# Kernel tuning notes

Hardware: AMD Instinct MI355X
Metric: run time of the kernel (lower is better)

## Reference

```python
import jax, jax.numpy as jnp
import numpy as np

EPS = 1e-5  # PNA std-aggregator epsilon
N_NODES, N_EDGES, F_DIM, N_LAYERS = 50000, 800000, 64, 3


def setup_inputs() -> dict:
    key = jax.random.key(0)
    ks = jax.random.split(key, 6)
    x = jax.random.normal(ks[0], (N_NODES, F_DIM), jnp.float32)
    edge_index = jax.random.randint(ks[1], (2, N_EDGES), 0, N_NODES, jnp.int32)
    # Per-layer parameters, stacked on a leading layer axis.
    pre_w = jax.random.normal(ks[2], (N_LAYERS, 2 * F_DIM, F_DIM), jnp.float32) / np.sqrt(2 * F_DIM).astype(np.float32)
    pre_b = jnp.zeros((N_LAYERS, F_DIM), jnp.float32)
    post_w = jax.random.normal(ks[3], (N_LAYERS, 13 * F_DIM, F_DIM), jnp.float32) / np.sqrt(13 * F_DIM).astype(np.float32)
    post_b = jnp.zeros((N_LAYERS, F_DIM), jnp.float32)
    lin_w = jax.random.normal(ks[4], (N_LAYERS, F_DIM, F_DIM), jnp.float32) / np.sqrt(F_DIM).astype(np.float32)
    lin_b = jnpp = jnp.zeros((N_LAYERS, F_DIM), jnp.float32)
    return dict(x=x, edge_index=edge_index, pre_w=pre_w, pre_b=pre_b,
                post_w=post_w, post_b=post_b, lin_w=lin_w, lin_b=lin_b)


def reference(x, edge_index, pre_w, pre_b, post_w, post_b, lin_w, lin_b):
    src, dst = edge_index[0], edge_index[1]
    n = x.shape[0]
    # In-degree of aggregation targets (clamped to >=1, as in PyG DegreeScalerAggregation).
    deg = jax.ops.segment_sum(jnp.ones_like(dst, dtype=x.dtype), dst, num_segments=n)
    has_edge = (deg > 0)[:, None]
    deg_c = jnp.maximum(deg, 1.0)[:, None]              # [N,1]
    log_deg = jnp.log(deg_c + 1.0)                      # [N,1]
    avg_log = jnp.mean(log_deg)
    amp = log_deg / avg_log                              # amplification scaler
    att = avg_log / log_deg                              # attenuation scaler

    h = x
    for l in range(pre_w.shape[0]):
        # message: pre_nn(cat([x_i, x_j]))  -> [E, F]
        m = jnp.concatenate([h[dst], h[src]], axis=-1) @ pre_w[l] + pre_b[l]
        # fused multi-aggregator scatter-reduce per target node
        s1 = jax.ops.segment_sum(m, dst, num_segments=n)
        s2 = jax.ops.segment_sum(m * m, dst, num_segments=n)
        mean = s1 / deg_c
        std = jnp.sqrt(jax.nn.relu(s2 / deg_c - mean * mean) + EPS)
        mx = jnp.where(has_edge, jax.ops.segment_max(m, dst, num_segments=n), 0.0)
        mn = jnp.where(has_edge, jax.ops.segment_min(m, dst, num_segments=n), 0.0)
        agg = jnp.concatenate([mean, mx, mn, std], axis=-1)        # [N, 4F]
        scaled = jnp.concatenate([agg, agg * amp, agg * att], -1)  # [N, 12F]
        # post_nn(cat([x, scaled])) then final lin, plus residual shortcut
        out = jnp.concatenate([h, scaled], axis=-1) @ post_w[l] + post_b[l]
        out = out @ lin_w[l] + lin_b[l]
        h = out + h
    return h
```

## Files before the change

kernel.cpp:

```cpp
#include <hip/hip_runtime.h>
#include <math.h>

#define EPSV 1e-5f
#define EPB3 4096
#define NBP 256
#define CAP 6144
#define CAPS (CAP + 768)

typedef short s16x8 __attribute__((ext_vector_type(8)));
typedef float f32x4 __attribute__((ext_vector_type(4)));
typedef unsigned short u16;
typedef unsigned short u16x4 __attribute__((ext_vector_type(4)));

#define MFMA(a, b, c) __builtin_amdgcn_mfma_f32_16x16x32_bf16(a, b, c, 0, 0, 0)

__device__ inline u16 f2bf(float f) {
    unsigned u = __float_as_uint(f);
    return (u16)((u + 0x7FFF + ((u >> 16) & 1)) >> 16);
}
__device__ inline float bf2f(u16 h) { return __uint_as_float(((unsigned)h) << 16); }

__device__ inline void split8(const float4& a, const float4& b, s16x8& hv, s16x8& lv) {
    float f[8] = {a.x, a.y, a.z, a.w, b.x, b.y, b.z, b.w};
#pragma unroll
    for (int i = 0; i < 8; ++i) {
        u16 h = f2bf(f[i]);
        hv[i] = (short)h;
        lv[i] = (short)f2bf(f[i] - bf2f(h));
    }
}


__global__ void k_wprep(const float* __restrict__ pre_w, const float* __restrict__ post_w,
                        const float* __restrict__ post_b, const float* __restrict__ lin_w,
                        const float* __restrict__ lin_b, u16* __restrict__ WpT_hi,
                        u16* __restrict__ WpT_lo, u16* __restrict__ WT_hi,
                        u16* __restrict__ WT_lo, float* __restrict__ bpp,
                        int* __restrict__ bucketCur, float* __restrict__ lsum) {
    int l = blockIdx.y, bx = blockIdx.x, t = threadIdx.x;
    if (bx < 320) {
        int k = bx, j = t;
        int third = j >> 6, c = j & 63;
        float out = 0.f;
        int r = -1;
        if (k < 64) r = (third == 0) ? k : -1;
        else        r = 64 + third * 256 + (k - 64);
        if (r >= 0) {
            const float* pw = post_w + (size_t)(l * 832 + r) * 64;
            const float* lw = lin_w + (size_t)l * 64 * 64;
            float s = 0.f;
            for (int kk = 0; kk < 64; ++kk) s += pw[kk] * lw[kk * 64 + c];
            out = s;
        }
        u16 h = f2bf(out);
        size_t o = ((size_t)l * 192 + j) * 320 + k;
        WT_hi[o] = h;
        WT_lo[o] = f2bf(out - bf2f(h));
    } else if (bx < 448) {
        if (t < 64) {
            int c = bx - 320, k = t;
            float v = pre_w[(size_t)l * 8192 + (size_t)(k + (c >= 64 ? 64 : 0)) * 64 + (c & 63)];
            u16 h = f2bf(v);
            size_t o = ((size_t)l * 128 + c) * 64 + k;
            WpT_hi[o] = h;
            WpT_lo[o] = f2bf(v - bf2f(h));
        }
    } else if (bx == 448) {
        if (t < 64) {
            int c = t;
            const float* pb = post_b + l * 64;
            const float* lw = lin_w + (size_t)l * 64 * 64;
            float s = lin_b[l * 64 + c];
            for (int k = 0; k < 64; ++k) s += pb[k] * lw[k * 64 + c];
            bpp[l * 64 + c] = s;
        }
    } else if (l == 0) {
        int i = (bx - 449) * 192 + t;
        if (i < NBP) bucketCur[i] = 0;
        if (i == 0) *lsum = 0.f;
    }
}

__global__ __launch_bounds__(512) void k_bucket3(const int* __restrict__ src,
                                                 const int* __restrict__ dst, int E,
                                                 int* __restrict__ bucketCursor,
                                                 unsigned* __restrict__ edgeTmp) {
    __shared__ int cnt[NBP], loff[NBP], lpos[NBP], gbase[NBP], sbuf[NBP];
    __shared__ unsigned stage[EPB3];
    int t = threadIdx.x;
    int base = blockIdx.x * EPB3;
    int cntE = min(EPB3, E - base);
    if (t < NBP) cnt[t] = 0;
    __syncthreads();
    unsigned ed[8];
#pragma unroll
    for (int j = 0; j < 8; ++j) {
        int idx = j * 512 + t;
        if (idx < cntE) {
            int e = base + idx;
            unsigned s = (unsigned)src[e];
            unsigned d = (unsigned)dst[e];
            ed[j] = ((d >> 8) << 24) | ((d & 255u) << 16) | s;
            atomicAdd(&cnt[d >> 8], 1);
        } else ed[j] = 0xFFFFFFFFu;
    }
    __syncthreads();
    if (t < NBP) sbuf[t] = cnt[t];
    __syncthreads();
    for (int o = 1; o < NBP; o <<= 1) {
        int v = 0;
        if (t < NBP && t >= o) v = sbuf[t - o];
        __syncthreads();
        if (t < NBP) sbuf[t] += v;
        __syncthreads();
    }
    if (t < NBP) {
        loff[t] = sbuf[t] - cnt[t];
        lpos[t] = sbuf[t] - cnt[t];
        gbase[t] = (cnt[t] > 0) ? atomicAdd(&bucketCursor[t], cnt[t]) : 0;
    }
    __syncthreads();
#pragma unroll
    for (int j = 0; j < 8; ++j) {
        if (ed[j] != 0xFFFFFFFFu) {
            int b = ed[j] >> 24;
            int p = atomicAdd(&lpos[b], 1);
            stage[p] = ed[j];
        }
    }
    __syncthreads();
    for (int i = t; i < cntE; i += 512) {
        unsigned pr = stage[i];
        int b = pr >> 24;
        int pos = gbase[b] + (i - loff[b]);
        if (pos < CAP) edgeTmp[(size_t)b * CAP + pos] = pr;
    }
}

__global__ __launch_bounds__(512) void k_csort2(const unsigned* __restrict__ edgeTmp,
                                                const int* __restrict__ bucketCur,
                                                int* __restrict__ deg,
                                                int* __restrict__ offs,
                                                float* __restrict__ lsum,
                                                u16* __restrict__ srcSorted,
                                                int N, int E, int NB) {
    __shared__ int scnt[NBP], sbuf[NBP], lcur[NBP], lofs[NBP];
    __shared__ float fred[256];
    __shared__ u16 stageSrc[CAPS];
    __shared__ int cntPs;
    int b = blockIdx.x, t = threadIdx.x;
    int n0 = b << 8;
    int nodes = min(256, N - n0);
    if (t < NBP) { lcur[t] = 0; scnt[t] = 0; }
    __syncthreads();
    int cnt = min(bucketCur[b], CAP);
    const unsigned* ebase = edgeTmp + (size_t)b * CAP;
    for (int i = t; i < cnt; i += 512) atomicAdd(&lcur[(ebase[i] >> 16) & 255], 1);
    __syncthreads();
    float ls = 0.f;
    int d = 0, dP = 0;
    if (t < nodes) {
        d = lcur[t];
        deg[n0 + t] = d;
        ls = logf(fmaxf((float)d, 1.f) + 1.f);
        dP = (d + 3) & ~3;
    }
    if (t < 256) fred[t] = ls;
    if (t < NBP) sbuf[t] = dP;
    __syncthreads();
    for (int o = 1; o < NBP; o <<= 1) {
        int v = 0;
        if (t < NBP && t >= o) v = sbuf[t - o];
        __syncthreads();
        if (t < NBP) sbuf[t] += v;
        __syncthreads();
    }
    if (t < NBP) lofs[t] = sbuf[t] - dP;
    if (t < nodes) offs[n0 + t] = b * CAPS + (sbuf[t] - dP);
    if (t == NBP - 1) cntPs = sbuf[t];
    __syncthreads();
    for (int o = 128; o > 0; o >>= 1) {
        if (t < o) fred[t] += fred[t + o];
        __syncthreads();
    }
    if (t == 0) atomicAdd(lsum, fred[0]);
    for (int i = t; i < cnt; i += 512) {
        unsigned p = ebase[i];
        int dl = (p >> 16) & 255;
        int r = atomicAdd(&scnt[dl], 1);
        stageSrc[lofs[dl] + r] = (u16)(p & 0xFFFFu);
    }
    __syncthreads();
    if (t < nodes && (d & 3)) {
        int lp = lofs[t];
        u16 lastv = stageSrc[lp + d - 1];
        for (int k = d; k < dP; ++k) stageSrc[lp + k] = lastv;
    }
    __syncthreads();
    int cntP = cntPs;
    for (int i = t; i < cntP; i += 512) srcSorted[(size_t)b * CAPS + i] = stageSrc[i];
}


__global__ __launch_bounds__(256) void k_gemm1(const float* __restrict__ h,
                                               const u16* __restrict__ WpT_hi,
                                               const u16* __restrict__ WpT_lo,
                                               const float* __restrict__ pre_b,
                                               u16* __restrict__ Ph, u16* __restrict__ Qh,
                                               int M) {
    __shared__ u16 Ah[64 * 72], Al[64 * 72];
    __shared__ u16 Bh[128 * 72], Bl[128 * 72];
    int t = threadIdx.x, wid = t >> 6, lane = t & 63;
    int rows0 = blockIdx.x * 64;
    int quad = lane >> 4, l16 = lane & 15;
    int wm = wid & 1, wn = wid >> 1;

#pragma unroll
    for (int it = 0; it < 2; ++it) {
        int task = it * 256 + t;
        int r = task >> 3, seg = task & 7;
        int row = rows0 + r;
        float4 v0 = make_float4(0.f, 0.f, 0.f, 0.f), v1 = v0;
        if (row < M) {
            v0 = *(const float4*)&h[(size_t)row * 64 + seg * 8];
            v1 = *(const float4*)&h[(size_t)row * 64 + seg * 8 + 4];
        }
        s16x8 hv, lv;
        split8(v0, v1, hv, lv);
        *(s16x8*)&Ah[r * 72 + seg * 8] = hv;
        *(s16x8*)&Al[r * 72 + seg * 8] = lv;
    }
#pragma unroll
    for (int it = 0; it < 4; ++it) {
        int task = it * 256 + t;
        int c = task >> 3, seg = task & 7;
        *(s16x8*)&Bh[c * 72 + seg * 8] = *(const s16x8*)&WpT_hi[(size_t)c * 64 + seg * 8];
        *(s16x8*)&Bl[c * 72 + seg * 8] = *(const s16x8*)&WpT_lo[(size_t)c * 64 + seg * 8];
    }
    __syncthreads();

    f32x4 acc[2][4];
#pragma unroll
    for (int mt = 0; mt < 2; ++mt)
#pragma unroll
        for (int tt = 0; tt < 4; ++tt) acc[mt][tt] = (f32x4){0.f, 0.f, 0.f, 0.f};

#pragma unroll
    for (int c = 0; c < 2; ++c) {
        s16x8 ah[2], al[2];
#pragma unroll
        for (int mt = 0; mt < 2; ++mt) {
            int r = wm * 32 + mt * 16 + l16;
            ah[mt] = *(s16x8*)&Ah[r * 72 + c * 32 + quad * 8];
            al[mt] = *(s16x8*)&Al[r * 72 + c * 32 + quad * 8];
        }
#pragma unroll
        for (int tt = 0; tt < 4; ++tt) {
            int cc = wn * 64 + tt * 16 + l16;
            s16x8 bh = *(s16x8*)&Bh[cc * 72 + c * 32 + quad * 8];
            s16x8 bl = *(s16x8*)&Bl[cc * 72 + c * 32 + quad * 8];
#pragma unroll
            for (int mt = 0; mt < 2; ++mt) {
                acc[mt][tt] = MFMA(ah[mt], bh, acc[mt][tt]);
                acc[mt][tt] = MFMA(ah[mt], bl, acc[mt][tt]);
                if (wn == 0) acc[mt][tt] = MFMA(al[mt], bh, acc[mt][tt]);
            }
        }
    }

#pragma unroll
    for (int mt = 0; mt < 2; ++mt)
#pragma unroll
        for (int tt = 0; tt < 4; ++tt) {
            int col = wn * 64 + tt * 16 + l16;
#pragma unroll
            for (int r = 0; r < 4; ++r) {
                int row = rows0 + wm * 32 + mt * 16 + quad * 4 + r;
                if (row >= M) continue;
                float v = acc[mt][tt][r];
                if (col < 64) Ph[(size_t)row * 64 + col] = f2bf(v + pre_b[col]);
                else          Qh[(size_t)row * 64 + (col - 64)] = f2bf(v);
            }
        }
}

__global__ __launch_bounds__(256) void k_agg(const u16* __restrict__ Ph,
                                             const u16* __restrict__ Qh,
                                             const int* __restrict__ offs,
                                             const int* __restrict__ degp,
                                             const u16* __restrict__ ss,
                                             u16* __restrict__ AGGh, int N) {
    int w = threadIdx.x >> 6, lane = threadIdx.x & 63;
    int g = lane >> 4;
    int f4b = (lane & 15) << 3;
    int node = blockIdx.x * 16 + w * 4 + g;
    int nc = min(node, N - 1);
    int beg = offs[nc];
    int d = (node < N) ? degp[nc] : 0;
    int dP = (d + 3) & ~3;
    int end = beg + dP;
    int mdP = dP;
    mdP = max(mdP, __shfl_xor(mdP, 16));
    mdP = max(mdP, __shfl_xor(mdP, 32));
    int trips = mdP >> 2;

    float sum0 = 0.f, sum1 = 0.f, sum2 = 0.f, sum3 = 0.f;
    float sq0 = 0.f, sq1 = 0.f, sq2 = 0.f, sq3 = 0.f;
    float mx0 = -3.4e38f, mx1 = -3.4e38f, mx2 = -3.4e38f, mx3 = -3.4e38f;
    float mn0 = 3.4e38f, mn1 = 3.4e38f, mn2 = 3.4e38f, mn3 = 3.4e38f;

    const char* qbase = (const char*)Qh;

#define ACC4(LO, HI)                                                        \
    {                                                                       \
        float q0 = __uint_as_float((LO) << 16);                             \
        float q1 = __uint_as_float((LO) & 0xFFFF0000u);                     \
        float q2 = __uint_as_float((HI) << 16);                             \
        float q3 = __uint_as_float((HI) & 0xFFFF0000u);                     \
        sum0 += q0; sq0 = fmaf(q0, q0, sq0);                                \
        mx0 = fmaxf(mx0, q0); mn0 = fminf(mn0, q0);                         \
        sum1 += q1; sq1 = fmaf(q1, q1, sq1);                                \
        mx1 = fmaxf(mx1, q1); mn1 = fminf(mn1, q1);                         \
        sum2 += q2; sq2 = fmaf(q2, q2, sq2);                                \
        mx2 = fmaxf(mx2, q2); mn2 = fminf(mn2, q2);                         \
        sum3 += q3; sq3 = fmaf(q3, q3, sq3);                                \
        mx3 = fmaxf(mx3, q3); mn3 = fminf(mn3, q3);                         \
    }

    int e = beg;
    for (int it = 0; it < trips; ++it, e += 4) {
        if (e < end) {
            uint2 sw = *(const uint2*)(ss + e);
            unsigned a0 = ((sw.x & 0xFFFFu) << 7) | (unsigned)f4b;
            unsigned a1 = ((sw.x >> 16) << 7) | (unsigned)f4b;
            unsigned a2 = ((sw.y & 0xFFFFu) << 7) | (unsigned)f4b;
            unsigned a3 = ((sw.y >> 16) << 7) | (unsigned)f4b;
            uint2 qa = *(const uint2*)(qbase + a0);
            uint2 qb = *(const uint2*)(qbase + a1);
            uint2 qc = *(const uint2*)(qbase + a2);
            uint2 qd = *(const uint2*)(qbase + a3);
            ACC4(qa.x, qa.y);
            ACC4(qb.x, qb.y);
            ACC4(qc.x, qc.y);
            ACC4(qd.x, qd.y);
        }
    }
#undef ACC4

    if (d & 3) {
        unsigned sl = ss[beg + d - 1];
        uint2 ql = *(const uint2*)(qbase + ((sl << 7) | (unsigned)f4b));
        float padf = (float)(dP - d);
        float qL0 = __uint_as_float(ql.x << 16);
        float qL1 = __uint_as_float(ql.x & 0xFFFF0000u);
        float qL2 = __uint_as_float(ql.y << 16);
        float qL3 = __uint_as_float(ql.y & 0xFFFF0000u);
        float t0 = padf * qL0, t1 = padf * qL1, t2 = padf * qL2, t3 = padf * qL3;
        sum0 -= t0; sq0 = fmaf(-t0, qL0, sq0);
        sum1 -= t1; sq1 = fmaf(-t1, qL1, sq1);
        sum2 -= t2; sq2 = fmaf(-t2, qL2, sq2);
        sum3 -= t3; sq3 = fmaf(-t3, qL3, sq3);
    }

    float dc = fmaxf((float)d, 1.f);
    float inv = 1.0f / dc;
    float e0 = sum0 * inv, e1 = sum1 * inv, e2 = sum2 * inv, e3 = sum3 * inv;
    float sd0 = sqrtf(fmaxf(fmaf(-e0, e0, sq0 * inv), 0.f) + EPSV);
    float sd1 = sqrtf(fmaxf(fmaf(-e1, e1, sq1 * inv), 0.f) + EPSV);
    float sd2 = sqrtf(fmaxf(fmaf(-e2, e2, sq2 * inv), 0.f) + EPSV);
    float sd3 = sqrtf(fmaxf(fmaf(-e3, e3, sq3 * inv), 0.f) + EPSV);

    uint2 pw = *(const uint2*)((const char*)Ph + (((unsigned)nc << 7) | (unsigned)f4b));
    float p0 = __uint_as_float(pw.x << 16), p1 = __uint_as_float(pw.x & 0xFFFF0000u);
    float p2 = __uint_as_float(pw.y << 16), p3 = __uint_as_float(pw.y & 0xFFFF0000u);

    bool he = d > 0;
    float m0 = he ? p0 + e0 : 0.f, m1 = he ? p1 + e1 : 0.f;
    float m2 = he ? p2 + e2 : 0.f, m3 = he ? p3 + e3 : 0.f;
    float X0 = he ? p0 + mx0 : 0.f, X1 = he ? p1 + mx1 : 0.f;
    float X2 = he ? p2 + mx2 : 0.f, X3 = he ? p3 + mx3 : 0.f;
    float n0 = he ? p0 + mn0 : 0.f, n1 = he ? p1 + mn1 : 0.f;
    float n2 = he ? p2 + mn2 : 0.f, n3 = he ? p3 + mn3 : 0.f;

    if (node < N) {
        u16* out = (u16*)((char*)AGGh + (((unsigned)node << 9) | (unsigned)f4b));
        *(u16x4*)(out)       = (u16x4){f2bf(m0), f2bf(m1), f2bf(m2), f2bf(m3)};
        *(u16x4*)(out + 64)  = (u16x4){f2bf(X0), f2bf(X1), f2bf(X2), f2bf(X3)};
        *(u16x4*)(out + 128) = (u16x4){f2bf(n0), f2bf(n1), f2bf(n2), f2bf(n3)};
        *(u16x4*)(out + 192) = (u16x4){f2bf(sd0), f2bf(sd1), f2bf(sd2), f2bf(sd3)};
    }
}

__global__ __launch_bounds__(512) void k_gemm2(const float* __restrict__ hIn,
                                               const u16* __restrict__ AGGh,
                                               const u16* __restrict__ WT_hi,
                                               const u16* __restrict__ WT_lo,
                                               const float* __restrict__ bpp,
                                               const int* __restrict__ degp,
                                               const float* __restrict__ lsum,
                                               float* __restrict__ hOut,
                                               int doNext,
                                               const u16* __restrict__ WpN_hi,
                                               const u16* __restrict__ WpN_lo,
                                               const float* __restrict__ pre_bN,
                                               u16* __restrict__ PhN,
                                               u16* __restrict__ QhN, int M) {
    __shared__ u16 Ah[128 * 40], Al[128 * 40];
    __shared__ u16 Bh[192 * 40], Bl[192 * 40];
    int t = threadIdx.x, wid = t >> 6, lane = t & 63;
    int rows0 = blockIdx.x * 128;
    int quad = lane >> 4, l16 = lane & 15;
    int wm = wid & 3, wn = wid >> 2;

    f32x4 acc[2][6];
#pragma unroll
    for (int mt = 0; mt < 2; ++mt)
#pragma unroll
        for (int tt = 0; tt < 6; ++tt) acc[mt][tt] = (f32x4){0.f, 0.f, 0.f, 0.f};

#pragma unroll
    for (int chunk = 0; chunk < 2; ++chunk) {
        {
            int r = t >> 2, seg = t & 3;
            int row = rows0 + r;
            float4 v0 = make_float4(0.f, 0.f, 0.f, 0.f), v1 = v0;
            if (row < M) {
                v0 = *(const float4*)&hIn[(size_t)row * 64 + chunk * 32 + seg * 8];
                v1 = *(const float4*)&hIn[(size_t)row * 64 + chunk * 32 + seg * 8 + 4];
            }
            s16x8 hv, lv;
            split8(v0, v1, hv, lv);
            *(s16x8*)&Ah[r * 40 + seg * 8] = hv;
            *(s16x8*)&Al[r * 40 + seg * 8] = lv;
        }
        if (t < 256) {
            int c = t >> 2, seg = t & 3;
            int k0g = chunk * 32;
            *(s16x8*)&Bh[c * 40 + seg * 8] = *(const s16x8*)&WT_hi[(size_t)c * 320 + k0g + seg * 8];
            *(s16x8*)&Bl[c * 40 + seg * 8] = *(const s16x8*)&WT_lo[(size_t)c * 320 + k0g + seg * 8];
        }
        __syncthreads();

        s16x8 ah[2], al[2];
#pragma unroll
        for (int mt = 0; mt < 2; ++mt) {
            int r = wm * 32 + mt * 16 + l16;
            ah[mt] = *(s16x8*)&Ah[r * 40 + quad * 8];
            al[mt] = *(s16x8*)&Al[r * 40 + quad * 8];
        }
#pragma unroll
        for (int cg = 0; cg < 2; ++cg) {
            int cc = wn * 32 + cg * 16 + l16;
            s16x8 bh = *(s16x8*)&Bh[cc * 40 + quad * 8];
            s16x8 bl = *(s16x8*)&Bl[cc * 40 + quad * 8];
#pragma unroll
            for (int mt = 0; mt < 2; ++mt) {
                acc[mt][cg] = MFMA(ah[mt], bh, acc[mt][cg]);
                acc[mt][cg] = MFMA(al[mt], bh, acc[mt][cg]);
                acc[mt][cg] = MFMA(ah[mt], bl, acc[mt][cg]);
            }
        }
        __syncthreads();
    }

    for (int chunk = 0; chunk < 8; ++chunk) {
        {
            int r = t >> 2, seg = t & 3;
            int row = rows0 + r;
            s16x8 v = (s16x8){0, 0, 0, 0, 0, 0, 0, 0};
            if (row < M) v = *(const s16x8*)&AGGh[(size_t)row * 256 + chunk * 32 + seg * 8];
            *(s16x8*)&Ah[r * 40 + seg * 8] = v;
        }
        {
            int k0g = 64 + chunk * 32;
#pragma unroll
            for (int it = 0; it < 2; ++it) {
                int task = it * 512 + t;
                if (task < 768) {
                    int c = task >> 2, seg = task & 3;
                    *(s16x8*)&Bh[c * 40 + seg * 8] = *(const s16x8*)&WT_hi[(size_t)c * 320 + k0g + seg * 8];
                    *(s16x8*)&Bl[c * 40 + seg * 8] = *(const s16x8*)&WT_lo[(size_t)c * 320 + k0g + seg * 8];
                }
            }
        }
        __syncthreads();

        s16x8 ah[2];
#pragma unroll
        for (int mt = 0; mt < 2; ++mt) {
            int r = wm * 32 + mt * 16 + l16;
            ah[mt] = *(s16x8*)&Ah[r * 40 + quad * 8];
        }
#pragma unroll
        for (int tt = 0; tt < 6; ++tt) {
            int cc = wn * 32 + (tt & 1) * 16 + (tt >> 1) * 64 + l16;
// ... 63 lines not shown
                            Al[rl * 40 + lc] = f2bf(v - bf2f(hi));
                        }
                    }
            }
            __syncthreads();

            s16x8 ah[2], al[2];
#pragma unroll
            for (int mt = 0; mt < 2; ++mt) {
                int r = wm * 32 + mt * 16 + l16;
                ah[mt] = *(s16x8*)&Ah[r * 40 + quad * 8];
                al[mt] = *(s16x8*)&Al[r * 40 + quad * 8];
            }
#pragma unroll
            for (int tt = 0; tt < 4; ++tt) {
                int cc = wn * 64 + tt * 16 + l16;
                s16x8 bh = *(s16x8*)&Bh[cc * 40 + quad * 8];
                s16x8 bl = *(s16x8*)&Bl[cc * 40 + quad * 8];
#pragma unroll
                for (int mt = 0; mt < 2; ++mt) {
                    acc2[mt][tt] = MFMA(ah[mt], bh, acc2[mt][tt]);
                    acc2[mt][tt] = MFMA(ah[mt], bl, acc2[mt][tt]);
                    if (wn == 0) acc2[mt][tt] = MFMA(al[mt], bh, acc2[mt][tt]);
                }
            }
            __syncthreads();
        }

#pragma unroll
        for (int mt = 0; mt < 2; ++mt)
#pragma unroll
            for (int tt = 0; tt < 4; ++tt) {
                int col = wn * 64 + tt * 16 + l16;
#pragma unroll
                for (int r = 0; r < 4; ++r) {
                    int row = rows0 + wm * 32 + mt * 16 + quad * 4 + r;
                    if (row >= M) continue;
                    float v = acc2[mt][tt][r];
                    if (col < 64) PhN[(size_t)row * 64 + col] = f2bf(v + pre_bN[col]);
                    else          QhN[(size_t)row * 64 + (col - 64)] = f2bf(v);
                }
            }
    }
}


extern "C" void kernel_launch(void* const* d_in, const int* in_sizes, int n_in,
                              void* d_out, int out_size, void* d_ws, size_t ws_size,
                              hipStream_t stream) {
    const float* x      = (const float*)d_in[0];
    const int*   ei     = (const int*)d_in[1];
    const float* pre_w  = (const float*)d_in[2];
    const float* pre_b  = (const float*)d_in[3];
    const float* post_w = (const float*)d_in[4];
    const float* post_b = (const float*)d_in[5];
    const float* lin_w  = (const float*)d_in[6];
    const float* lin_b  = (const float*)d_in[7];

    const int N = in_sizes[0] / 64;
    const int E = in_sizes[1] / 2;
    const int L = in_sizes[2] / (128 * 64);

    const int* srcIdx = ei;
    const int* dstIdx = ei + E;

    char* ws = (char*)d_ws;
    size_t off = 0;
    auto alloc = [&](size_t bytes) {
        void* p = ws + off;
        off += (bytes + 255) & ~(size_t)255;
        return p;
    };
    int*      deg        = (int*)alloc((size_t)N * 4);
    int*      offs       = (int*)alloc((size_t)(N + 1) * 4);
    u16*      srcSorted  = (u16*)alloc((size_t)NBP * CAPS * 2);
    unsigned* edgeTmp    = (unsigned*)alloc((size_t)NBP * CAP * 4);
    int*      bucketCur  = (int*)alloc(NBP * 4);
    float*    lsum       = (float*)alloc(256);
    u16*      WpT_hi     = (u16*)alloc((size_t)L * 128 * 64 * 2);
    u16*      WpT_lo     = (u16*)alloc((size_t)L * 128 * 64 * 2);
    u16*      WT_hi      = (u16*)alloc((size_t)L * 192 * 320 * 2);
    u16*      WT_lo      = (u16*)alloc((size_t)L * 192 * 320 * 2);
    float*    bpp        = (float*)alloc((size_t)L * 64 * 4);
    u16*      Ph         = (u16*)alloc((size_t)N * 64 * 2);
    u16*      Qh         = (u16*)alloc((size_t)N * 64 * 2);
    u16*      AGGh       = (u16*)alloc((size_t)N * 256 * 2);
    float*    hA         = (float*)alloc((size_t)N * 64 * 4);
    float*    hB         = (float*)alloc((size_t)N * 64 * 4);
    (void)ws_size;

    int NB = (N + 255) >> 8;
    int NB1 = (E + EPB3 - 1) / EPB3;
    int initBlk = (NBP + 191) / 192;

    k_wprep<<<dim3(449 + initBlk, L), 192, 0, stream>>>(
        pre_w, post_w, post_b, lin_w, lin_b, WpT_hi, WpT_lo, WT_hi, WT_lo, bpp,
        bucketCur, lsum);
    k_bucket3<<<NB1, 512, 0, stream>>>(srcIdx, dstIdx, E, bucketCur, edgeTmp);
    k_csort2<<<NB, 512, 0, stream>>>(edgeTmp, bucketCur, deg, offs, lsum,
                                     srcSorted, N, E, NB);

    int gblk = (N + 63) / 64;
    int gblk2 = (N + 127) / 128;
    k_gemm1<<<gblk, 256, 0, stream>>>(x, WpT_hi, WpT_lo, pre_b, Ph, Qh, N);

    const float* hIn = x;
    float* hbuf[2] = {hA, hB};
    for (int l = 0; l < L; ++l) {
        float* hOut = (l == L - 1) ? (float*)d_out : hbuf[l & 1];
        int dn = (l < L - 1) ? 1 : 0;
        int ln = dn ? (l + 1) : 0;
        k_agg<<<(N + 15) / 16, 256, 0, stream>>>(Ph, Qh, offs, deg, srcSorted, AGGh, N);
        k_gemm2<<<gblk2, 512, 0, stream>>>(hIn, AGGh,
                                           WT_hi + (size_t)l * 192 * 320,
                                           WT_lo + (size_t)l * 192 * 320,
                                           bpp + (size_t)l * 64,
                                           deg, lsum, hOut, dn,
                                           WpT_hi + (size_t)ln * 128 * 64,
                                           WpT_lo + (size_t)ln * 128 * 64,
                                           pre_b + (size_t)ln * 64,
                                           Ph, Qh, N);
        hIn = hOut;
    }
}
```

Measured before the change: 277.0 us.

## Fuse aggregation into per-layer GEMM kernel and merge preprocessing launches

Each layer's edge aggregation is folded into the post-GEMM kernel, so every 128-node block gathers its own neighbors, writes the aggregated features, then runs the GEMM. The Ph/Qh buffers are double-buffered because the next layer's projections are written while other blocks may still be reading the current ones. Weight prep and edge bucketing are merged into one launch, and CSR sort and the first projection GEMM into another, with memsets replacing the init blocks. This cuts launch count and inter-kernel gaps, but the gather now shares a kernel with the GEMM, which may raise register and LDS pressure and lower occupancy. It also relies on AGGh rows written within a block being visible to that same block's GEMM.

```diff
diff --git a/kernel.cpp b/kernel.cpp
--- a/kernel.cpp
+++ b/kernel.cpp
@@ -10,7 +10,6 @@
 typedef short s16x8 __attribute__((ext_vector_type(8)));
 typedef float f32x4 __attribute__((ext_vector_type(4)));
 typedef unsigned short u16;
-typedef unsigned short u16x4 __attribute__((ext_vector_type(4)));
 
 #define MFMA(a, b, c) __builtin_amdgcn_mfma_f32_16x16x32_bf16(a, b, c, 0, 0, 0)
 
@@ -30,32 +29,99 @@
     }
 }
 
-
-__global__ void k_wprep(const float* __restrict__ pre_w, const float* __restrict__ post_w,
-                        const float* __restrict__ post_b, const float* __restrict__ lin_w,
-                        const float* __restrict__ lin_b, u16* __restrict__ WpT_hi,
-                        u16* __restrict__ WpT_lo, u16* __restrict__ WT_hi,
-                        u16* __restrict__ WT_lo, float* __restrict__ bpp,
-                        int* __restrict__ bucketCur, float* __restrict__ lsum) {
-    int l = blockIdx.y, bx = blockIdx.x, t = threadIdx.x;
+__device__ inline uint4 pack8(const float* v) {
+    uint4 r;
+    r.x = (unsigned)f2bf(v[0]) | ((unsigned)f2bf(v[1]) << 16);
+    r.y = (unsigned)f2bf(v[2]) | ((unsigned)f2bf(v[3]) << 16);
+    r.z = (unsigned)f2bf(v[4]) | ((unsigned)f2bf(v[5]) << 16);
+    r.w = (unsigned)f2bf(v[6]) | ((unsigned)f2bf(v[7]) << 16);
+    return r;
+}
+
+__global__ __launch_bounds__(512) void k_pre1(
+    const int* __restrict__ src, const int* __restrict__ dst, int E,
+    int* __restrict__ bucketCursor, unsigned* __restrict__ edgeTmp,
+    const float* __restrict__ pre_w, const float* __restrict__ post_w,
+    const float* __restrict__ post_b, const float* __restrict__ lin_w,
+    const float* __restrict__ lin_b, u16* __restrict__ WpT_hi,
+    u16* __restrict__ WpT_lo, u16* __restrict__ WT_hi, u16* __restrict__ WT_lo,
+    float* __restrict__ bpp, int NB1) {
+    __shared__ int cnt[NBP], loff[NBP], lpos[NBP], gbase[NBP], sbuf[NBP];
+    __shared__ unsigned stage[EPB3];
+    int t = threadIdx.x;
+    if ((int)blockIdx.x < NB1) {
+        int base = blockIdx.x * EPB3;
+        int cntE = min(EPB3, E - base);
+        if (t < NBP) cnt[t] = 0;
+        __syncthreads();
+        unsigned ed[8];
+#pragma unroll
+        for (int j = 0; j < 8; ++j) {
+            int idx = j * 512 + t;
+            if (idx < cntE) {
+                int e = base + idx;
+                unsigned s = (unsigned)src[e];
+                unsigned d = (unsigned)dst[e];
+                ed[j] = ((d >> 8) << 24) | ((d & 255u) << 16) | s;
+                atomicAdd(&cnt[d >> 8], 1);
+            } else ed[j] = 0xFFFFFFFFu;
+        }
+        __syncthreads();
+        if (t < NBP) sbuf[t] = cnt[t];
+        __syncthreads();
+        for (int o = 1; o < NBP; o <<= 1) {
+            int v = 0;
+            if (t < NBP && t >= o) v = sbuf[t - o];
+            __syncthreads();
+            if (t < NBP) sbuf[t] += v;
+            __syncthreads();
+        }
+        if (t < NBP) {
+            loff[t] = sbuf[t] - cnt[t];
+            lpos[t] = sbuf[t] - cnt[t];
+            gbase[t] = (cnt[t] > 0) ? atomicAdd(&bucketCursor[t], cnt[t]) : 0;
+        }
+        __syncthreads();
+#pragma unroll
+        for (int j = 0; j < 8; ++j) {
+            if (ed[j] != 0xFFFFFFFFu) {
+                int b = ed[j] >> 24;
+                int p = atomicAdd(&lpos[b], 1);
+                stage[p] = ed[j];
+            }
+        }
+        __syncthreads();
+        for (int i = t; i < cntE; i += 512) {
+            unsigned pr = stage[i];
+            int b = pr >> 24;
+            int pos = gbase[b] + (i - loff[b]);
+            if (pos < CAP) edgeTmp[(size_t)b * CAP + pos] = pr;
+        }
+        return;
+    }
+    int wq = blockIdx.x - NB1;
+    int l = wq / 449;
+    int bx = wq - l * 449;
     if (bx < 320) {
-        int k = bx, j = t;
-        int third = j >> 6, c = j & 63;
-        float out = 0.f;
-        int r = -1;
-        if (k < 64) r = (third == 0) ? k : -1;
-        else        r = 64 + third * 256 + (k - 64);
-        if (r >= 0) {
-            const float* pw = post_w + (size_t)(l * 832 + r) * 64;
-            const float* lw = lin_w + (size_t)l * 64 * 64;
-            float s = 0.f;
-            for (int kk = 0; kk < 64; ++kk) s += pw[kk] * lw[kk * 64 + c];
-            out = s;
-        }
-        u16 h = f2bf(out);
-        size_t o = ((size_t)l * 192 + j) * 320 + k;
-        WT_hi[o] = h;
-        WT_lo[o] = f2bf(out - bf2f(h));
+        if (t < 192) {
+            int k = bx, j = t;
+            int third = j >> 6, c = j & 63;
+            float out = 0.f;
+            int r = -1;
+            if (k < 64) r = (third == 0) ? k : -1;
+            else        r = 64 + third * 256 + (k - 64);
+            if (r >= 0) {
+                const float* pw = post_w + (size_t)(l * 832 + r) * 64;
+                const float* lw = lin_w + (size_t)l * 64 * 64;
+                float s = 0.f;
+                for (int kk = 0; kk < 64; ++kk) s += pw[kk] * lw[kk * 64 + c];
+                out = s;
+            }
+            u16 h = f2bf(out);
+            size_t o = ((size_t)l * 192 + j) * 320 + k;
+            WT_hi[o] = h;
+            WT_lo[o] = f2bf(out - bf2f(h));
+        }
     } else if (bx < 448) {
         if (t < 64) {
             int c = bx - 320, k = t;
@@ -65,7 +131,7 @@
             WpT_hi[o] = h;
             WpT_lo[o] = f2bf(v - bf2f(h));
         }
-    } else if (bx == 448) {
+    } else {
         if (t < 64) {
             int c = t;
             const float* pb = post_b + l * 64;
@@ -74,343 +140,258 @@
             for (int k = 0; k < 64; ++k) s += pb[k] * lw[k * 64 + c];
             bpp[l * 64 + c] = s;
         }
-    } else if (l == 0) {
-        int i = (bx - 449) * 192 + t;
-        if (i < NBP) bucketCur[i] = 0;
-        if (i == 0) *lsum = 0.f;
     }
 }
 
-__global__ __launch_bounds__(512) void k_bucket3(const int* __restrict__ src,
-                                                 const int* __restrict__ dst, int E,
-                                                 int* __restrict__ bucketCursor,
-                                                 unsigned* __restrict__ edgeTmp) {
-    __shared__ int cnt[NBP], loff[NBP], lpos[NBP], gbase[NBP], sbuf[NBP];
-    __shared__ unsigned stage[EPB3];
+__global__ __launch_bounds__(512) void k_pre2(
+    const unsigned* __restrict__ edgeTmp, const int* __restrict__ bucketCur,
+    int* __restrict__ deg, int* __restrict__ offs, float* __restrict__ lsum,
+    u16* __restrict__ srcSorted,
+    const float* __restrict__ x, const u16* __restrict__ WpT_hi,
+    const u16* __restrict__ WpT_lo, const float* __restrict__ pre_b,
+    u16* __restrict__ Ph, u16* __restrict__ Qh,
+    int N, int E, int NB) {
+    __shared__ __align__(16) char smem[55296];
     int t = threadIdx.x;
-    int base = blockIdx.x * EPB3;
-    int cntE = min(EPB3, E - base);
-    if (t < NBP) cnt[t] = 0;
-    __syncthreads();
-    unsigned ed[8];
-#pragma unroll
-    for (int j = 0; j < 8; ++j) {
-        int idx = j * 512 + t;
-        if (idx < cntE) {
-            int e = base + idx;
-            unsigned s = (unsigned)src[e];
-            unsigned d = (unsigned)dst[e];
-            ed[j] = ((d >> 8) << 24) | ((d & 255u) << 16) | s;
-            atomicAdd(&cnt[d >> 8], 1);
-        } else ed[j] = 0xFFFFFFFFu;
-    }
-    __syncthreads();
-    if (t < NBP) sbuf[t] = cnt[t];
-    __syncthreads();
-    for (int o = 1; o < NBP; o <<= 1) {
-        int v = 0;
-        if (t < NBP && t >= o) v = sbuf[t - o];
-        __syncthreads();
-        if (t < NBP) sbuf[t] += v;
-        __syncthreads();
-    }
-    if (t < NBP) {
-        loff[t] = sbuf[t] - cnt[t];
-        lpos[t] = sbuf[t] - cnt[t];
-        gbase[t] = (cnt[t] > 0) ? atomicAdd(&bucketCursor[t], cnt[t]) : 0;
-    }
-    __syncthreads();
-#pragma unroll
-    for (int j = 0; j < 8; ++j) {
-        if (ed[j] != 0xFFFFFFFFu) {
-            int b = ed[j] >> 24;
-            int p = atomicAdd(&lpos[b], 1);
-            stage[p] = ed[j];
-        }
-    }
-    __syncthreads();
-    for (int i = t; i < cntE; i += 512) {
-        unsigned pr = stage[i];
-        int b = pr >> 24;
-        int pos = gbase[b] + (i - loff[b]);
-        if (pos < CAP) edgeTmp[(size_t)b * CAP + pos] = pr;
-    }
-}
-
-__global__ __launch_bounds__(512) void k_csort2(const unsigned* __restrict__ edgeTmp,
-                                                const int* __restrict__ bucketCur,
-                                                int* __restrict__ deg,
-                                                int* __restrict__ offs,
-                                                float* __restrict__ lsum,
-                                                u16* __restrict__ srcSorted,
-                                                int N, int E, int NB) {
-    __shared__ int scnt[NBP], sbuf[NBP], lcur[NBP], lofs[NBP];
-    __shared__ float fred[256];
-    __shared__ u16 stageSrc[CAPS];
-    __shared__ int cntPs;
-    int b = blockIdx.x, t = threadIdx.x;
-    int n0 = b << 8;
-    int nodes = min(256, N - n0);
-    if (t < NBP) { lcur[t] = 0; scnt[t] = 0; }
-    __syncthreads();
-    int cnt = min(bucketCur[b], CAP);
-    const unsigned* ebase = edgeTmp + (size_t)b * CAP;
-    for (int i = t; i < cnt; i += 512) atomicAdd(&lcur[(ebase[i] >> 16) & 255], 1);
-    __syncthreads();
-    float ls = 0.f;
-    int d = 0, dP = 0;
-    if (t < nodes) {
-        d = lcur[t];
-        deg[n0 + t] = d;
-        ls = logf(fmaxf((float)d, 1.f) + 1.f);
-        dP = (d + 3) & ~3;
-    }
-    if (t < 256) fred[t] = ls;
-    if (t < NBP) sbuf[t] = dP;
-    __syncthreads();
-    for (int o = 1; o < NBP; o <<= 1) {
-        int v = 0;
-        if (t < NBP && t >= o) v = sbuf[t - o];
-        __syncthreads();
-        if (t < NBP) sbuf[t] += v;
-        __syncthreads();
-    }
-    if (t < NBP) lofs[t] = sbuf[t] - dP;
-    if (t < nodes) offs[n0 + t] = b * CAPS + (sbuf[t] - dP);
-    if (t == NBP - 1) cntPs = sbuf[t];
-    __syncthreads();
-    for (int o = 128; o > 0; o >>= 1) {
-        if (t < o) fred[t] += fred[t + o];
-        __syncthreads();
-    }
-    if (t == 0) atomicAdd(lsum, fred[0]);
-    for (int i = t; i < cnt; i += 512) {
-        unsigned p = ebase[i];
-        int dl = (p >> 16) & 255;
-        int r = atomicAdd(&scnt[dl], 1);
-        stageSrc[lofs[dl] + r] = (u16)(p & 0xFFFFu);
-    }
-    __syncthreads();
-    if (t < nodes && (d & 3)) {
-        int lp = lofs[t];
-        u16 lastv = stageSrc[lp + d - 1];
-        for (int k = d; k < dP; ++k) stageSrc[lp + k] = lastv;
-    }
-    __syncthreads();
-    int cntP = cntPs;
-    for (int i = t; i < cntP; i += 512) srcSorted[(size_t)b * CAPS + i] = stageSrc[i];
-}
-
-
-__global__ __launch_bounds__(256) void k_gemm1(const float* __restrict__ h,
-                                               const u16* __restrict__ WpT_hi,
-                                               const u16* __restrict__ WpT_lo,
-                                               const float* __restrict__ pre_b,
-                                               u16* __restrict__ Ph, u16* __restrict__ Qh,
-                                               int M) {
-    __shared__ u16 Ah[64 * 72], Al[64 * 72];
-    __shared__ u16 Bh[128 * 72], Bl[128 * 72];
-    int t = threadIdx.x, wid = t >> 6, lane = t & 63;
-    int rows0 = blockIdx.x * 64;
+    if ((int)blockIdx.x < NB) {
+        int* scnt = (int*)smem;
+        int* sbuf = (int*)(smem + 1024);
+        int* lcur = (int*)(smem + 2048);
+        int* lofs = (int*)(smem + 3072);
+        float* fred = (float*)(smem + 4096);
+        u16* stageSrc = (u16*)(smem + 5120);
+        int* cntPs = (int*)(smem + 5120 + CAPS * 2);
+        int b = blockIdx.x;
+        int n0 = b << 8;
+        int nodes = min(256, N - n0);
+        if (t < NBP) { lcur[t] = 0; scnt[t] = 0; }
+        __syncthreads();
+        int cnt = min(bucketCur[b], CAP);
+        const unsigned* ebase = edgeTmp + (size_t)b * CAP;
+        for (int i = t; i < cnt; i += 512) atomicAdd(&lcur[(ebase[i] >> 16) & 255], 1);
+        __syncthreads();
+        float ls = 0.f;
+        int d = 0, dP = 0;
+        if (t < nodes) {
+            d = lcur[t];
+            deg[n0 + t] = d;
+            ls = logf(fmaxf((float)d, 1.f) + 1.f);
+            dP = (d + 3) & ~3;
+        }
+        if (t < 256) fred[t] = ls;
+        if (t < NBP) sbuf[t] = dP;
+        __syncthreads();
+        for (int o = 1; o < NBP; o <<= 1) {
+            int v = 0;
+            if (t < NBP && t >= o) v = sbuf[t - o];
+            __syncthreads();
+            if (t < NBP) sbuf[t] += v;
+            __syncthreads();
+        }
+        if (t < NBP) lofs[t] = sbuf[t] - dP;
+        if (t < nodes) offs[n0 + t] = b * CAPS + (sbuf[t] - dP);
+        if (t == NBP - 1) *cntPs = sbuf[t];
+        __syncthreads();
+        for (int o = 128; o > 0; o >>= 1) {
+            if (t < o) fred[t] += fred[t + o];
+            __syncthreads();
+        }
+        if (t == 0) atomicAdd(lsum, fred[0]);
+        for (int i = t; i < cnt; i += 512) {
+            unsigned p = ebase[i];
+            int dl = (p >> 16) & 255;
+            int r = atomicAdd(&scnt[dl], 1);
+            stageSrc[lofs[dl] + r] = (u16)(p & 0xFFFFu);
+        }
+        __syncthreads();
+        if (t < nodes && (d & 3)) {
+            int lp = lofs[t];
+            u16 lastv = stageSrc[lp + d - 1];
+            for (int k = d; k < dP; ++k) stageSrc[lp + k] = lastv;
+        }
+        __syncthreads();
+        int cntP = *cntPs;
+        for (int i = t; i < cntP; i += 512) srcSorted[(size_t)b * CAPS + i] = stageSrc[i];
+        return;
+    }
+    u16* Ah = (u16*)smem;
+    u16* Al = (u16*)(smem + 9216);
+    u16* Bh = (u16*)(smem + 18432);
+    u16* Bl = (u16*)(smem + 36864);
+    int rows0 = ((int)blockIdx.x - NB) * 64;
+    int wid = t >> 6, lane = t & 63;
     int quad = lane >> 4, l16 = lane & 15;
     int wm = wid & 1, wn = wid >> 1;
-
-#pragma unroll
-    for (int it = 0; it < 2; ++it) {
-        int task = it * 256 + t;
-        int r = task >> 3, seg = task & 7;
-        int row = rows0 + r;
-        float4 v0 = make_float4(0.f, 0.f, 0.f, 0.f), v1 = v0;
-        if (row < M) {
-            v0 = *(const float4*)&h[(size_t)row * 64 + seg * 8];
-            v1 = *(const float4*)&h[(size_t)row * 64 + seg * 8 + 4];
-        }
-        s16x8 hv, lv;
-        split8(v0, v1, hv, lv);
-        *(s16x8*)&Ah[r * 72 + seg * 8] = hv;
-        *(s16x8*)&Al[r * 72 + seg * 8] = lv;
-    }
-#pragma unroll
-    for (int it = 0; it < 4; ++it) {
-        int task = it * 256 + t;
-        int c = task >> 3, seg = task & 7;
-        *(s16x8*)&Bh[c * 72 + seg * 8] = *(const s16x8*)&WpT_hi[(size_t)c * 64 + seg * 8];
-        *(s16x8*)&Bl[c * 72 + seg * 8] = *(const s16x8*)&WpT_lo[(size_t)c * 64 + seg * 8];
+    if (t < 256) {
+#pragma unroll
+        for (int it = 0; it < 2; ++it) {
+            int task = it * 256 + t;
+            int r = task >> 3, seg = task & 7;
+            int row = rows0 + r;
+            float4 v0 = make_float4(0.f, 0.f, 0.f, 0.f), v1 = v0;
+            if (row < N) {
+                v0 = *(const float4*)&x[(size_t)row * 64 + seg * 8];
+                v1 = *(const float4*)&x[(size_t)row * 64 + seg * 8 + 4];
+            }
+            s16x8 hv, lv;
+            split8(v0, v1, hv, lv);
+            *(s16x8*)&Ah[r * 72 + seg * 8] = hv;
+            *(s16x8*)&Al[r * 72 + seg * 8] = lv;
+        }
+#pragma unroll
+        for (int it = 0; it < 4; ++it) {
+            int task = it * 256 + t;
+            int c = task >> 3, seg = task & 7;
+            *(s16x8*)&Bh[c * 72 + seg * 8] = *(const s16x8*)&WpT_hi[(size_t)c * 64 + seg * 8];
+            *(s16x8*)&Bl[c * 72 + seg * 8] = *(const s16x8*)&WpT_lo[(size_t)c * 64 + seg * 8];
+        }
     }
     __syncthreads();
-
-    f32x4 acc[2][4];
-#pragma unroll
-    for (int mt = 0; mt < 2; ++mt)
-#pragma unroll
-        for (int tt = 0; tt < 4; ++tt) acc[mt][tt] = (f32x4){0.f, 0.f, 0.f, 0.f};
-
-#pragma unroll
-    for (int c = 0; c < 2; ++c) {
-        s16x8 ah[2], al[2];
-#pragma unroll
-        for (int mt = 0; mt < 2; ++mt) {
-            int r = wm * 32 + mt * 16 + l16;
-            ah[mt] = *(s16x8*)&Ah[r * 72 + c * 32 + quad * 8];
-            al[mt] = *(s16x8*)&Al[r * 72 + c * 32 + quad * 8];
-        }
-#pragma unroll
-        for (int tt = 0; tt < 4; ++tt) {
-            int cc = wn * 64 + tt * 16 + l16;
-            s16x8 bh = *(s16x8*)&Bh[cc * 72 + c * 32 + quad * 8];
-            s16x8 bl = *(s16x8*)&Bl[cc * 72 + c * 32 + quad * 8];
+    if (t < 256) {
+        f32x4 acc[2][4];
+#pragma unroll
+        for (int mt = 0; mt < 2; ++mt)
+#pragma unroll
+            for (int tt = 0; tt < 4; ++tt) acc[mt][tt] = (f32x4){0.f, 0.f, 0.f, 0.f};
+#pragma unroll
+        for (int c = 0; c < 2; ++c) {
+            s16x8 ah[2], al[2];
 #pragma unroll
             for (int mt = 0; mt < 2; ++mt) {
-                acc[mt][tt] = MFMA(ah[mt], bh, acc[mt][tt]);
-                acc[mt][tt] = MFMA(ah[mt], bl, acc[mt][tt]);
-                if (wn == 0) acc[mt][tt] = MFMA(al[mt], bh, acc[mt][tt]);
-            }
-        }
-    }
-
-#pragma unroll
-    for (int mt = 0; mt < 2; ++mt)
-#pragma unroll
-        for (int tt = 0; tt < 4; ++tt) {
-            int col = wn * 64 + tt * 16 + l16;
-#pragma unroll
-            for (int r = 0; r < 4; ++r) {
-                int row = rows0 + wm * 32 + mt * 16 + quad * 4 + r;
-                if (row >= M) continue;
-                float v = acc[mt][tt][r];
-                if (col < 64) Ph[(size_t)row * 64 + col] = f2bf(v + pre_b[col]);
-                else          Qh[(size_t)row * 64 + (col - 64)] = f2bf(v);
-            }
-        }
+                int r = wm * 32 + mt * 16 + l16;
+                ah[mt] = *(s16x8*)&Ah[r * 72 + c * 32 + quad * 8];
+                al[mt] = *(s16x8*)&Al[r * 72 + c * 32 + quad * 8];
+            }
+#pragma unroll
+            for (int tt = 0; tt < 4; ++tt) {
+                int cc = wn * 64 + tt * 16 + l16;
+                s16x8 bh = *(s16x8*)&Bh[cc * 72 + c * 32 + quad * 8];
+                s16x8 bl = *(s16x8*)&Bl[cc * 72 + c * 32 + quad * 8];
+#pragma unroll
+                for (int mt = 0; mt < 2; ++mt) {
+                    acc[mt][tt] = MFMA(ah[mt], bh, acc[mt][tt]);
+                    acc[mt][tt] = MFMA(ah[mt], bl, acc[mt][tt]);
+                    if (wn == 0) acc[mt][tt] = MFMA(al[mt], bh, acc[mt][tt]);
+                }
+            }
+        }
+#pragma unroll
+        for (int mt = 0; mt < 2; ++mt)
+#pragma unroll
+            for (int tt = 0; tt < 4; ++tt) {
+                int col = wn * 64 + tt * 16 + l16;
+#pragma unroll
+                for (int r = 0; r < 4; ++r) {
+                    int row = rows0 + wm * 32 + mt * 16 + quad * 4 + r;
+                    if (row >= N) continue;
+                    float v = acc[mt][tt][r];
+                    if (col < 64) Ph[(size_t)row * 64 + col] = f2bf(v + pre_b[col]);
+                    else          Qh[(size_t)row * 64 + (col - 64)] = f2bf(v);
+                }
+            }
+    }
 }
 
-__global__ __launch_bounds__(256) void k_agg(const u16* __restrict__ Ph,
-                                             const u16* __restrict__ Qh,
-                                             const int* __restrict__ offs,
-                                             const int* __restrict__ degp,
-                                             const u16* __restrict__ ss,
-                                             u16* __restrict__ AGGh, int N) {
-    int w = threadIdx.x >> 6, lane = threadIdx.x & 63;
-    int g = lane >> 4;
-    int f4b = (lane & 15) << 3;
-    int node = blockIdx.x * 16 + w * 4 + g;
-    int nc = min(node, N - 1);
-    int beg = offs[nc];
-    int d = (node < N) ? degp[nc] : 0;
-    int dP = (d + 3) & ~3;
-    int end = beg + dP;
-    int mdP = dP;
-    mdP = max(mdP, __shfl_xor(mdP, 16));
-    mdP = max(mdP, __shfl_xor(mdP, 32));
-    int trips = mdP >> 2;
-
-    float sum0 = 0.f, sum1 = 0.f, sum2 = 0.f, sum3 = 0.f;
-    float sq0 = 0.f, sq1 = 0.f, sq2 = 0.f, sq3 = 0.f;
-    float mx0 = -3.4e38f, mx1 = -3.4e38f, mx2 = -3.4e38f, mx3 = -3.4e38f;
-    float mn0 = 3.4e38f, mn1 = 3.4e38f, mn2 = 3.4e38f, mn3 = 3.4e38f;
-
-    const char* qbase = (const char*)Qh;
-
-#define ACC4(LO, HI)                                                        \
-    {                                                                       \
-        float q0 = __uint_as_float((LO) << 16);                             \
-        float q1 = __uint_as_float((LO) & 0xFFFF0000u);                     \
-        float q2 = __uint_as_float((HI) << 16);                             \
-        float q3 = __uint_as_float((HI) & 0xFFFF0000u);                     \
-        sum0 += q0; sq0 = fmaf(q0, q0, sq0);                                \
-        mx0 = fmaxf(mx0, q0); mn0 = fminf(mn0, q0);                         \
-        sum1 += q1; sq1 = fmaf(q1, q1, sq1);                                \
-        mx1 = fmaxf(mx1, q1); mn1 = fminf(mn1, q1);                         \
-        sum2 += q2; sq2 = fmaf(q2, q2, sq2);                                \
-        mx2 = fmaxf(mx2, q2); mn2 = fminf(mn2, q2);                         \
-        sum3 += q3; sq3 = fmaf(q3, q3, sq3);                                \
-        mx3 = fmaxf(mx3, q3); mn3 = fminf(mn3, q3);                         \
-    }
-
-    int e = beg;
-    for (int it = 0; it < trips; ++it, e += 4) {
-        if (e < end) {
-            uint2 sw = *(const uint2*)(ss + e);
-            unsigned a0 = ((sw.x & 0xFFFFu) << 7) | (unsigned)f4b;
-            unsigned a1 = ((sw.x >> 16) << 7) | (unsigned)f4b;
-            unsigned a2 = ((sw.y & 0xFFFFu) << 7) | (unsigned)f4b;
-            unsigned a3 = ((sw.y >> 16) << 7) | (unsigned)f4b;
-            uint2 qa = *(const uint2*)(qbase + a0);
-            uint2 qb = *(const uint2*)(qbase + a1);
-            uint2 qc = *(const uint2*)(qbase + a2);
-            uint2 qd = *(const uint2*)(qbase + a3);
-            ACC4(qa.x, qa.y);
-            ACC4(qb.x, qb.y);
-            ACC4(qc.x, qc.y);
-            ACC4(qd.x, qd.y);
-        }
-    }
-#undef ACC4
-
-    if (d & 3) {
-        unsigned sl = ss[beg + d - 1];
-        uint2 ql = *(const uint2*)(qbase + ((sl << 7) | (unsigned)f4b));
-        float padf = (float)(dP - d);
-        float qL0 = __uint_as_float(ql.x << 16);
-        float qL1 = __uint_as_float(ql.x & 0xFFFF0000u);
-        float qL2 = __uint_as_float(ql.y << 16);
-        float qL3 = __uint_as_float(ql.y & 0xFFFF0000u);
-        float t0 = padf * qL0, t1 = padf * qL1, t2 = padf * qL2, t3 = padf * qL3;
-        sum0 -= t0; sq0 = fmaf(-t0, qL0, sq0);
-        sum1 -= t1; sq1 = fmaf(-t1, qL1, sq1);
-        sum2 -= t2; sq2 = fmaf(-t2, qL2, sq2);
-        sum3 -= t3; sq3 = fmaf(-t3, qL3, sq3);
-    }
-
-    float dc = fmaxf((float)d, 1.f);
-    float inv = 1.0f / dc;
-    float e0 = sum0 * inv, e1 = sum1 * inv, e2 = sum2 * inv, e3 = sum3 * inv;
-    float sd0 = sqrtf(fmaxf(fmaf(-e0, e0, sq0 * inv), 0.f) + EPSV);
-    float sd1 = sqrtf(fmaxf(fmaf(-e1, e1, sq1 * inv), 0.f) + EPSV);
-    float sd2 = sqrtf(fmaxf(fmaf(-e2, e2, sq2 * inv), 0.f) + EPSV);
-    float sd3 = sqrtf(fmaxf(fmaf(-e3, e3, sq3 * inv), 0.f) + EPSV);
-
-    uint2 pw = *(const uint2*)((const char*)Ph + (((unsigned)nc << 7) | (unsigned)f4b));
-    float p0 = __uint_as_float(pw.x << 16), p1 = __uint_as_float(pw.x & 0xFFFF0000u);
-    float p2 = __uint_as_float(pw.y << 16), p3 = __uint_as_float(pw.y & 0xFFFF0000u);
-
-    bool he = d > 0;
-    float m0 = he ? p0 + e0 : 0.f, m1 = he ? p1 + e1 : 0.f;
-    float m2 = he ? p2 + e2 : 0.f, m3 = he ? p3 + e3 : 0.f;
-    float X0 = he ? p0 + mx0 : 0.f, X1 = he ? p1 + mx1 : 0.f;
-    float X2 = he ? p2 + mx2 : 0.f, X3 = he ? p3 + mx3 : 0.f;
-    float n0 = he ? p0 + mn0 : 0.f, n1 = he ? p1 + mn1 : 0.f;
-    float n2 = he ? p2 + mn2 : 0.f, n3 = he ? p3 + mn3 : 0.f;
-
-    if (node < N) {
-        u16* out = (u16*)((char*)AGGh + (((unsigned)node << 9) | (unsigned)f4b));
-        *(u16x4*)(out)       = (u16x4){f2bf(m0), f2bf(m1), f2bf(m2), f2bf(m3)};
-        *(u16x4*)(out + 64)  = (u16x4){f2bf(X0), f2bf(X1), f2bf(X2), f2bf(X3)};
-        *(u16x4*)(out + 128) = (u16x4){f2bf(n0), f2bf(n1), f2bf(n2), f2bf(n3)};
-        *(u16x4*)(out + 192) = (u16x4){f2bf(sd0), f2bf(sd1), f2bf(sd2), f2bf(sd3)};
-    }
-}
-
-__global__ __launch_bounds__(512) void k_gemm2(const float* __restrict__ hIn,
-                                               const u16* __restrict__ AGGh,
-                                               const u16* __restrict__ WT_hi,
-                                               const u16* __restrict__ WT_lo,
-                                               const float* __restrict__ bpp,
-                                               const int* __restrict__ degp,
-                                               const float* __restrict__ lsum,
-                                               float* __restrict__ hOut,
-                                               int doNext,
-                                               const u16* __restrict__ WpN_hi,
-                                               const u16* __restrict__ WpN_lo,
-                                               const float* __restrict__ pre_bN,
-                                               u16* __restrict__ PhN,
-                                               u16* __restrict__ QhN, int M) {
+__global__ __launch_bounds__(512) void k_layer(
+    const float* __restrict__ hIn, const u16* __restrict__ Ph,
+    const u16* __restrict__ Qh, const int* __restrict__ offs,
+    const int* __restrict__ degp, const u16* __restrict__ ss,
+    u16* __restrict__ AGGh,
+    const u16* __restrict__ WT_hi, const u16* __restrict__ WT_lo,
+    const float* __restrict__ bpp, const float* __restrict__ lsum,
+    float* __restrict__ hOut, int doNext,
+    const u16* __restrict__ WpN_hi, const u16* __restrict__ WpN_lo,
+    const float* __restrict__ pre_bN, u16* __restrict__ PhN,
+    u16* __restrict__ QhN, int M) {
     __shared__ u16 Ah[128 * 40], Al[128 * 40];
     __shared__ u16 Bh[192 * 40], Bl[192 * 40];
     int t = threadIdx.x, wid = t >> 6, lane = t & 63;
     int rows0 = blockIdx.x * 128;
     int quad = lane >> 4, l16 = lane & 15;
     int wm = wid & 3, wn = wid >> 2;
+
+    {
+        int nloc = t >> 2;
+        int node = rows0 + nloc;
+        int fb = (t & 3) << 3;
+        int nc2 = min(node, M - 1);
+        int beg = offs[nc2];
+        int d = (node < M) ? degp[nc2] : 0;
+        int dP = (d + 3) & ~3;
+        float sum[16], sq[16], mx[16], mn[16];
+#pragma unroll
+        for (int i = 0; i < 16; ++i) {
+            sum[i] = 0.f; sq[i] = 0.f; mx[i] = -3.4e38f; mn[i] = 3.4e38f;
+        }
+        const u16* ssb = ss + beg;
+        for (int e0 = 0; e0 < dP; e0 += 4) {
+            uint2 sw = *(const uint2*)(ssb + e0);
+            unsigned sid[4] = {sw.x & 0xFFFFu, sw.x >> 16, sw.y & 0xFFFFu, sw.y >> 16};
+#pragma unroll
+            for (int j = 0; j < 4; ++j) {
+                const u16* qr = Qh + ((size_t)sid[j] << 6) + fb;
+                uint4 qa = *(const uint4*)qr;
+                uint4 qb = *(const uint4*)(qr + 32);
+                unsigned wd[8] = {qa.x, qa.y, qa.z, qa.w, qb.x, qb.y, qb.z, qb.w};
+#pragma unroll
+                for (int k = 0; k < 8; ++k) {
+                    float v0 = __uint_as_float(wd[k] << 16);
+                    float v1 = __uint_as_float(wd[k] & 0xFFFF0000u);
+                    sum[2 * k] += v0; sq[2 * k] = fmaf(v0, v0, sq[2 * k]);
+                    mx[2 * k] = fmaxf(mx[2 * k], v0); mn[2 * k] = fminf(mn[2 * k], v0);
+                    sum[2 * k + 1] += v1; sq[2 * k + 1] = fmaf(v1, v1, sq[2 * k + 1]);
+                    mx[2 * k + 1] = fmaxf(mx[2 * k + 1], v1); mn[2 * k + 1] = fminf(mn[2 * k + 1], v1);
+                }
+            }
+        }
+        if (d & 3) {
+            unsigned s = ssb[d - 1];
+            const u16* qr = Qh + ((size_t)s << 6) + fb;
+            uint4 qa = *(const uint4*)qr;
+            uint4 qb = *(const uint4*)(qr + 32);
+            unsigned wd[8] = {qa.x, qa.y, qa.z, qa.w, qb.x, qb.y, qb.z, qb.w};
+            float pf = (float)(dP - d);
+#pragma unroll
+            for (int k = 0; k < 8; ++k) {
+                float v0 = __uint_as_float(wd[k] << 16);
+                float v1 = __uint_as_float(wd[k] & 0xFFFF0000u);
+                float t0 = pf * v0, t1 = pf * v1;
+                sum[2 * k] -= t0; sq[2 * k] = fmaf(-t0, v0, sq[2 * k]);
+                sum[2 * k + 1] -= t1; sq[2 * k + 1] = fmaf(-t1, v1, sq[2 * k + 1]);
+            }
+        }
+        float dc = fmaxf((float)d, 1.f);
+        float inv = 1.f / dc;
+        const u16* pr = Ph + ((size_t)nc2 << 6) + fb;
+        uint4 pa = *(const uint4*)pr;
+        uint4 pb = *(const uint4*)(pr + 32);
+        unsigned pw[8] = {pa.x, pa.y, pa.z, pa.w, pb.x, pb.y, pb.z, pb.w};
+        bool he = d > 0;
+        float vmean[16], vmax[16], vmin[16], vstd[16];
+#pragma unroll
+        for (int k = 0; k < 8; ++k) {
+            float p0 = __uint_as_float(pw[k] << 16);
+            float p1 = __uint_as_float(pw[k] & 0xFFFF0000u);
+            int i0 = 2 * k, i1 = 2 * k + 1;
+            float e0 = sum[i0] * inv, e1 = sum[i1] * inv;
+            vstd[i0] = sqrtf(fmaxf(fmaf(-e0, e0, sq[i0] * inv), 0.f) + EPSV);
+            vstd[i1] = sqrtf(fmaxf(fmaf(-e1, e1, sq[i1] * inv), 0.f) + EPSV);
+            vmean[i0] = he ? p0 + e0 : 0.f;   vmean[i1] = he ? p1 + e1 : 0.f;
+            vmax[i0] = he ? p0 + mx[i0] : 0.f; vmax[i1] = he ? p1 + mx[i1] : 0.f;
+            vmin[i0] = he ? p0 + mn[i0] : 0.f; vmin[i1] = he ? p1 + mn[i1] : 0.f;
+        }
+        if (node < M) {
+            u16* ob = AGGh + ((size_t)node << 8);
+            *(uint4*)(ob + fb)            = pack8(vmean);
+            *(uint4*)(ob + fb + 32)       = pack8(vmean + 8);
+            *(uint4*)(ob + 64 + fb)       = pack8(vmax);
+            *(uint4*)(ob + 64 + fb + 32)  = pack8(vmax + 8);
+            *(uint4*)(ob + 128 + fb)      = pack8(vmin);
+            *(uint4*)(ob + 128 + fb + 32) = pack8(vmin + 8);
+            *(uint4*)(ob + 192 + fb)      = pack8(vstd);
+            *(uint4*)(ob + 192 + fb + 32) = pack8(vstd + 8);
+        }
+    }
 
     f32x4 acc[2][6];
 #pragma unroll
@@ -640,27 +621,34 @@
     u16*      WT_hi      = (u16*)alloc((size_t)L * 192 * 320 * 2);
     u16*      WT_lo      = (u16*)alloc((size_t)L * 192 * 320 * 2);
     float*    bpp        = (float*)alloc((size_t)L * 64 * 4);
-    u16*      Ph         = (u16*)alloc((size_t)N * 64 * 2);
-    u16*      Qh         = (u16*)alloc((size_t)N * 64 * 2);
+    u16*      Ph0        = (u16*)alloc((size_t)N * 64 * 2);
+    u16*      Qh0        = (u16*)alloc((size_t)N * 64 * 2);
+    u16*      Ph1        = (u16*)alloc((size_t)N * 64 * 2);
+    u16*      Qh1        = (u16*)alloc((size_t)N * 64 * 2);
     u16*      AGGh       = (u16*)alloc((size_t)N * 256 * 2);
     float*    hA         = (float*)alloc((size_t)N * 64 * 4);
     float*    hB         = (float*)alloc((size_t)N * 64 * 4);
     (void)ws_size;
 
+    u16* PhB[2] = {Ph0, Ph1};
+    u16* QhB[2] = {Qh0, Qh1};
+
     int NB = (N + 255) >> 8;
     int NB1 = (E + EPB3 - 1) / EPB3;
-    int initBlk = (NBP + 191) / 192;
-
-    k_wprep<<<dim3(449 + initBlk, L), 192, 0, stream>>>(
-        pre_w, post_w, post_b, lin_w, lin_b, WpT_hi, WpT_lo, WT_hi, WT_lo, bpp,
-        bucketCur, lsum);
-    k_bucket3<<<NB1, 512, 0, stream>>>(srcIdx, dstIdx, E, bucketCur, edgeTmp);
-    k_csort2<<<NB, 512, 0, stream>>>(edgeTmp, bucketCur, deg, offs, lsum,
-                                     srcSorted, N, E, NB);
-
     int gblk = (N + 63) / 64;
     int gblk2 = (N + 127) / 128;
-    k_gemm1<<<gblk, 256, 0, stream>>>(x, WpT_hi, WpT_lo, pre_b, Ph, Qh, N);
+
+    hipMemsetAsync(bucketCur, 0, NBP * 4, stream);
+    hipMemsetAsync(lsum, 0, 4, stream);
+
+    k_pre1<<<NB1 + 449 * L, 512, 0, stream>>>(
+        srcIdx, dstIdx, E, bucketCur, edgeTmp,
+        pre_w, post_w, post_b, lin_w, lin_b,
+        WpT_hi, WpT_lo, WT_hi, WT_lo, bpp, NB1);
+
+    k_pre2<<<NB + gblk, 512, 0, stream>>>(
+        edgeTmp, bucketCur, deg, offs, lsum, srcSorted,
+        x, WpT_hi, WpT_lo, pre_b, PhB[0], QhB[0], N, E, NB);
 
     const float* hIn = x;
     float* hbuf[2] = {hA, hB};
@@ -668,16 +656,16 @@
         float* hOut = (l == L - 1) ? (float*)d_out : hbuf[l & 1];
         int dn = (l < L - 1) ? 1 : 0;
         int ln = dn ? (l + 1) : 0;
-        k_agg<<<(N + 15) / 16, 256, 0, stream>>>(Ph, Qh, offs, deg, srcSorted, AGGh, N);
-        k_gemm2<<<gblk2, 512, 0, stream>>>(hIn, AGGh,
-                                           WT_hi + (size_t)l * 192 * 320,
-                                           WT_lo + (size_t)l * 192 * 320,
-                                           bpp + (size_t)l * 64,
-                                           deg, lsum, hOut, dn,
-                                           WpT_hi + (size_t)ln * 128 * 64,
-                                           WpT_lo + (size_t)ln * 128 * 64,
-                                           pre_b + (size_t)ln * 64,
-                                           Ph, Qh, N);
+        k_layer<<<gblk2, 512, 0, stream>>>(
+            hIn, PhB[l & 1], QhB[l & 1], offs, deg, srcSorted, AGGh,
+            WT_hi + (size_t)l * 192 * 320,
+            WT_lo + (size_t)l * 192 * 320,
+            bpp + (size_t)l * 64,
+            lsum, hOut, dn,
+            WpT_hi + (size_t)ln * 128 * 64,
+            WpT_lo + (size_t)ln * 128 * 64,
+            pre_b + (size_t)ln * 64,
+            PhB[(l + 1) & 1], QhB[(l + 1) & 1], N);
         hIn = hOut;
     }
 }
```

After: 305.7 us. 10.4% more time.
